# Optimization experiments

Hardware: AMD Instinct MI355X
Metric: run time of the kernel (lower is better)

The kernel has to match this reference:

```python
import jax, jax.numpy as jnp
import numpy as np

B, S, D = 2, 2048, 1024
H = 16
HD = D // H  # 64


def setup_inputs() -> dict:
    key = jax.random.key(0)
    ks = jax.random.split(key, 6)
    std = 1.0 / np.sqrt(D)
    x = jax.random.normal(ks[0], (B, S, D), dtype=jnp.float32)
    Wq = jax.random.uniform(ks[1], (D, D), jnp.float32, -std, std)
    Wk = jax.random.uniform(ks[2], (D, D), jnp.float32, -std, std)
    Wv = jax.random.uniform(ks[3], (D, D), jnp.float32, -std, std)
    Wo = jax.random.uniform(ks[4], (D, D), jnp.float32, -std, std)
    bo = jax.random.uniform(ks[5], (D,), jnp.float32, -std, std)
    return {"x": x, "Wq": Wq, "Wk": Wk, "Wv": Wv, "Wo": Wo, "bo": bo}


def reference(x, Wq, Wk, Wv, Wo, bo):
    b, n, _ = x.shape
    # project and split heads: [b, H, n, HD]
    def split_heads(y):
        return y.reshape(b, n, H, HD).transpose(0, 2, 1, 3)
    q = split_heads(jnp.einsum('bnd,ed->bne', x, Wq))
    k = split_heads(jnp.einsum('bnd,ed->bne', x, Wk))
    v = split_heads(jnp.einsum('bnd,ed->bne', x, Wv))
    scores = jnp.einsum('bhqd,bhkd->bhqk', q, k)
    causal = jnp.triu(jnp.ones((n, n), dtype=bool), k=1)
    # original masks with -inf BEFORE scaling; -inf/scale == -inf so math matches
    scores = jnp.where(causal, -jnp.inf, scores) / jnp.sqrt(jnp.asarray(HD, scores.dtype))
    attn = jax.nn.softmax(scores, axis=-1)
    ctx = jnp.einsum('bhqk,bhkd->bhqd', attn, v)
    ctx = ctx.transpose(0, 2, 1, 3).reshape(b, n, D)
    return jnp.einsum('bnd,ed->bne', ctx, Wo) + bo
```

## Files before the change

kernel.cpp:

```cpp
#include <hip/hip_runtime.h>

#define DEV __device__ __forceinline__

typedef __bf16 bf16x8 __attribute__((ext_vector_type(8)));
typedef float f32x4 __attribute__((ext_vector_type(4)));
typedef float f32x16 __attribute__((ext_vector_type(16)));
typedef unsigned u32x4 __attribute__((ext_vector_type(4)));

constexpr int S_LEN = 2048;
constexpr int DMODEL = 1024;
constexpr int NHEAD = 16;
constexpr int HDIM = 64;
constexpr int BATCH = 2;
constexpr int MROWS = BATCH * S_LEN;
constexpr float QSCALE = 0.125f * 1.44269504088896f;

DEV short f2bf(float x) {
  unsigned u = __builtin_bit_cast(unsigned, x);
  unsigned r = u + 0x7fffu + ((u >> 16) & 1u);
  return (short)(r >> 16);
}

#define MFMA16(a, b, c) __builtin_amdgcn_mfma_f32_16x16x32_bf16((a), (b), (c), 0, 0, 0)
#define MFMA32(a, b, c) __builtin_amdgcn_mfma_f32_32x32x16_bf16((a), (b), (c), 0, 0, 0)
#define GLL16(g, l)                                                                     \
  __builtin_amdgcn_global_load_lds((const __attribute__((address_space(1))) void*)(g),  \
                                   (__attribute__((address_space(3))) void*)(l), 16, 0, 0)

DEV unsigned cvt_pk_bf16(float a, float b) {
  unsigned r;
  asm("v_cvt_pk_bf16_f32 %0, %1, %2" : "=v"(r) : "v"(a), "v"(b));
  return r;
}
DEV void swap32(unsigned& a, unsigned& b) {
  asm("v_permlane32_swap_b32 %0, %1" : "+v"(a), "+v"(b));
}

__global__ void cvt_kernel(const float* __restrict__ in, short* __restrict__ out, int n) {
  int i = (blockIdx.x * blockDim.x + threadIdx.x) * 4;
  const int stride = gridDim.x * blockDim.x * 4;
  for (; i < n; i += stride) {
    float4 v = *(const float4*)&in[i];
    short4 r;
    r.x = f2bf(v.x);
    r.y = f2bf(v.y);
    r.z = f2bf(v.z);
    r.w = f2bf(v.w);
    *(short4*)&out[i] = r;
  }
}

__global__ void cvt_w4(const float* __restrict__ Wq, const float* __restrict__ Wk,
                       const float* __restrict__ Wv, const float* __restrict__ Wo,
                       short* __restrict__ out) {
  const float* src = blockIdx.y == 0 ? Wq : blockIdx.y == 1 ? Wk : blockIdx.y == 2 ? Wv : Wo;
  short* dst = out + (size_t)blockIdx.y * (DMODEL * DMODEL);
  int i = (blockIdx.x * blockDim.x + threadIdx.x) * 4;
  const int stride = gridDim.x * blockDim.x * 4;
  for (; i < DMODEL * DMODEL; i += stride) {
    float4 v = *(const float4*)&src[i];
    short4 r;
    r.x = f2bf(v.x);
    r.y = f2bf(v.y);
    r.z = f2bf(v.z);
    r.w = f2bf(v.w);
    *(short4*)&dst[i] = r;
  }
}

__global__ __launch_bounds__(256) void gemm_bt(const short* __restrict__ A,
                                               const short* __restrict__ Bt,
                                               short* __restrict__ outb,
                                               float* __restrict__ outf,
                                               const float* __restrict__ bias,
                                               const int mode) {
  constexpr int K = DMODEL;
  constexpr int N = DMODEL;
  constexpr size_t XN = (size_t)MROWS * DMODEL;
  __shared__ short As[2][128 * 64];
  __shared__ short Bs[2][128 * 64];
  const int tid = threadIdx.x;
  const int w = tid >> 6, l = tid & 63;
  const int lr = l & 15, lh = l >> 4;
  const int wr = w >> 1, wc = w & 1;
  const int tm = blockIdx.x, tn = blockIdx.y;

  const int srow = tid >> 3;
  const int ssl = tid & 7;
  const int ssg = ssl ^ (srow & 7);

  f32x4 acc[4][4] = {};

#define GSTAGE(KT, BUF)                                                             \
  {                                                                                 \
    _Pragma("unroll") for (int i = 0; i < 4; ++i) {                                 \
      const int row = i * 32 + srow;                                                \
      GLL16(A + (size_t)(tm * 128 + row) * K + (KT)*64 + ssg * 8,                   \
            &As[BUF][(i * 256 + w * 64) * 8]);                                      \
    }                                                                               \
    _Pragma("unroll") for (int i = 0; i < 4; ++i) {                                 \
      const int row = i * 32 + srow;                                                \
      GLL16(Bt + (size_t)(tn * 128 + row) * K + (KT)*64 + ssg * 8,                  \
            &Bs[BUF][(i * 256 + w * 64) * 8]);                                      \
    }                                                                               \
  }

  GSTAGE(0, 0);
  asm volatile("s_waitcnt vmcnt(0)" ::: "memory");
  __syncthreads();

  for (int kt = 0; kt < K / 64; ++kt) {
    const int buf = kt & 1;
    if (kt < K / 64 - 1) GSTAGE(kt + 1, buf ^ 1);

#pragma unroll
    for (int kh = 0; kh < 2; ++kh) {
      bf16x8 af[4], bfr[4];
#pragma unroll
      for (int mi = 0; mi < 4; ++mi) {
        const int row = wr * 64 + mi * 16 + lr;
        af[mi] = *(const bf16x8*)&As[buf][row * 64 + 8 * ((kh * 4 + lh) ^ (row & 7))];
      }
#pragma unroll
      for (int ni = 0; ni < 4; ++ni) {
        const int row = wc * 64 + ni * 16 + lr;
        bfr[ni] = *(const bf16x8*)&Bs[buf][row * 64 + 8 * ((kh * 4 + lh) ^ (row & 7))];
      }
#pragma unroll
      for (int mi = 0; mi < 4; ++mi)
#pragma unroll
        for (int ni = 0; ni < 4; ++ni)
          acc[mi][ni] = MFMA16(af[mi], bfr[ni], acc[mi][ni]);
    }

    asm volatile("s_waitcnt vmcnt(0)" ::: "memory");
    __syncthreads();
  }
#undef GSTAGE

  const int m0 = tm * 128 + wr * 64;
  const int n0 = tn * 128 + wc * 64;
  if (mode == 3) {
#pragma unroll
    for (int mi = 0; mi < 4; ++mi)
#pragma unroll
      for (int ni = 0; ni < 4; ++ni)
#pragma unroll
        for (int i = 0; i < 4; ++i) {
          const int m = m0 + mi * 16 + lh * 4 + i;
          const int e = n0 + ni * 16 + lr;
          outf[(size_t)m * N + e] = acc[mi][ni][i] + bias[e];
        }
  } else {
    const int sel = tn >> 3;
#pragma unroll
    for (int mi = 0; mi < 4; ++mi)
#pragma unroll
      for (int ni = 0; ni < 4; ++ni)
#pragma unroll
        for (int i = 0; i < 4; ++i) {
          const int m = m0 + mi * 16 + lh * 4 + i;
          const int e = n0 + ni * 16 + lr;
          const int ecol = e & (DMODEL - 1);
          const int b = m >> 11, n = m & (S_LEN - 1);
          const int h = ecol >> 6, d = ecol & (HDIM - 1);
          if (sel == 0)
            outb[((size_t)((b * NHEAD + h) * S_LEN + n)) * HDIM + d] =
                f2bf(acc[mi][ni][i] * QSCALE);
          else if (sel == 1)
            (outb + XN)[((size_t)((b * NHEAD + h) * S_LEN + n)) * HDIM + d] =
                f2bf(acc[mi][ni][i]);
          else
            (outb + 2 * XN)[((size_t)((b * NHEAD + h) * HDIM + d)) * S_LEN + n] =
                f2bf(acc[mi][ni][i]);
        }
  }
}

__global__ __launch_bounds__(256) void attn_kernel(const short* __restrict__ Qg,
                                                   const short* __restrict__ Kg,
                                                   const short* __restrict__ Vg,
                                                   short* __restrict__ ctx) {
  __shared__ alignas(16) short KV[4][8192];
  __shared__ float mls[4][32];
  const int tidx = threadIdx.x;
  const int s = tidx >> 6;
  const int l = tidx & 63;
  const int lq = l & 31;
  const int h5 = l >> 5;
  const int bid = blockIdx.x;
  const int xcd = bid & 7;
  const int j = bid >> 3;
  const int bh = xcd * 4 + (j >> 6);
  const int qi = 63 - (j & 63);
  const int qbase = qi * 32;
  const short* Qh = Qg + (size_t)bh * (S_LEN * HDIM);
  const short* Kh = Kg + (size_t)bh * (S_LEN * HDIM);
  const short* Vh = Vg + (size_t)bh * (HDIM * S_LEN);

  short* Kbase = &KV[s][0];
  short* Vbase = &KV[s][4096];
  const int r8 = l >> 3;
  const int sc = l & 7;

  bf16x8 qf[4];
#pragma unroll
  for (int cc = 0; cc < 4; ++cc)
    qf[cc] = *(const bf16x8*)&Qh[(size_t)(qbase + lq) * HDIM + cc * 16 + h5 * 8];

  f32x16 o0 = {}, o1 = {};
  float ll = 0.f;

  const int ntot = qi + 1;
  const int ts = (ntot * s) >> 2;
  const int te = (ntot * (s + 1)) >> 2;

#define STAGE(T, BUF)                                                              \
  {                                                                                \
    _Pragma("unroll") for (int i = 0; i < 4; ++i) {                                \
      const int R = i * 8 + r8;                                 \
      const int sg = sc ^ (R & 7);          \
      GLL16(Kh + (size_t)((T)*32 + R) * HDIM + sg * 8,                             \
            &Kbase[(BUF)*2048 + i * 512]);                                         \
      GLL16(Vh + (size_t)(2 * R + (sg >> 2)) * S_LEN + (T)*32 + (sg & 3) * 8,      \
            &Vbase[(BUF)*2048 + i * 512]);                                         \
    }                                                                              \
  }

  if (ts < te) STAGE(ts, 0);

  for (int t = ts; t < te; ++t) {
    const int buf = (t - ts) & 1;
    if (t + 1 < te) {
      STAGE(t + 1, buf ^ 1);
      asm volatile("s_waitcnt vmcnt(8)" ::: "memory");
    } else {
      asm volatile("s_waitcnt vmcnt(0)" ::: "memory");
    }
    const short* Ksb = &Kbase[buf * 2048];
    const short* Vsb = &Vbase[buf * 2048];

    bf16x8 kf[4];
#pragma unroll
    for (int cc = 0; cc < 4; ++cc)
      kf[cc] = *(const bf16x8*)&Ksb[lq * 64 + 8 * ((cc * 2 + h5) ^ (lq & 7))];
    f32x16 st = {};
    __builtin_amdgcn_s_setprio(1);
#pragma unroll
    for (int cc = 0; cc < 4; ++cc) st = MFMA32(kf[cc], qf[cc], st);
    __builtin_amdgcn_s_setprio(0);

    if (t == qi) {
#pragma unroll
      for (int rr = 0; rr < 16; ++rr) {
        const int crow = (rr & 3) + 8 * (rr >> 2) + 4 * h5;
        if (crow > lq) st[rr] = -__builtin_inff();
      }
    }

#pragma unroll
    for (int rr = 0; rr < 16; ++rr) {
      st[rr] = __builtin_amdgcn_exp2f(st[rr]);
      ll += st[rr];
    }

    unsigned a0 = cvt_pk_bf16(st[0], st[1]), b0 = cvt_pk_bf16(st[4], st[5]);
    unsigned a1 = cvt_pk_bf16(st[2], st[3]), b1 = cvt_pk_bf16(st[6], st[7]);
    unsigned a2 = cvt_pk_bf16(st[8], st[9]), b2 = cvt_pk_bf16(st[12], st[13]);
    unsigned a3 = cvt_pk_bf16(st[10], st[11]), b3 = cvt_pk_bf16(st[14], st[15]);
    swap32(a0, b0);
    swap32(a1, b1);
    swap32(a2, b2);
    swap32(a3, b3);
    const u32x4 pw0 = {a0, a1, b0, b1};
    const u32x4 pw1 = {a2, a3, b2, b3};
    const bf16x8 pa0 = __builtin_bit_cast(bf16x8, pw0);
    const bf16x8 pa1 = __builtin_bit_cast(bf16x8, pw1);

    const int R0 = lq >> 1, p0 = (lq & 1) * 4 + h5;
    const int R1 = 16 + (lq >> 1);
    const bf16x8 v00 = *(const bf16x8*)&Vsb[R0 * 64 + 8 * ((p0 + 0) ^ (R0 & 7))];
    const bf16x8 v01 = *(const bf16x8*)&Vsb[R0 * 64 + 8 * ((p0 + 2) ^ (R0 & 7))];
    const bf16x8 v10 = *(const bf16x8*)&Vsb[R1 * 64 + 8 * ((p0 + 0) ^ (R1 & 7))];
    const bf16x8 v11 = *(const bf16x8*)&Vsb[R1 * 64 + 8 * ((p0 + 2) ^ (R1 & 7))];
    __builtin_amdgcn_s_setprio(1);
    o0 = MFMA32(pa0, v00, o0);
    o1 = MFMA32(pa0, v10, o1);
    o0 = MFMA32(pa1, v01, o0);
    o1 = MFMA32(pa1, v11, o1);
    __builtin_amdgcn_s_setprio(0);
  }
#undef STAGE

  float* me = (float*)&KV[s][0];
#pragma unroll
  for (int rr = 0; rr < 16; ++rr) {
    const int crow = (rr & 3) + 8 * (rr >> 2) + 4 * h5;
    me[crow * 64 + lq] = o0[rr];
    me[crow * 64 + 32 + lq] = o1[rr];
  }
  ll += __shfl_xor(ll, 32);
  if (h5 == 0) mls[s][lq] = ll;
  __syncthreads();

  const float* om0 = (const float*)&KV[0][0];
  const float* om1 = (const float*)&KV[1][0];
  const float* om2 = (const float*)&KV[2][0];
  const float* om3 = (const float*)&KV[3][0];
  const int b = bh >> 4, h = bh & (NHEAD - 1);
  const int r2 = tidx >> 3;
  const int d0 = (tidx & 7) * 8;
  const float inv =
      __builtin_amdgcn_rcpf(mls[0][r2] + mls[1][r2] + mls[2][r2] + mls[3][r2]);
  const size_t base = (size_t)(b * S_LEN + qbase + r2) * DMODEL + h * HDIM + d0;
#pragma unroll
  for (int i = 0; i < 8; ++i) {
    const int o = r2 * 64 + d0 + i;
    const float v = (om0[o] + om1[o] + om2[o] + om3[o]) * inv;
    ctx[base + i] = f2bf(v);
  }
}

extern "C" void kernel_launch(void* const* d_in, const int* in_sizes, int n_in,
                              void* d_out, int out_size, void* d_ws, size_t ws_size,
                              hipStream_t stream) {
  const float* x = (const float*)d_in[0];
  const float* Wq = (const float*)d_in[1];
  const float* Wk = (const float*)d_in[2];
  const float* Wv = (const float*)d_in[3];
  const float* Wo = (const float*)d_in[4];
  const float* bo = (const float*)d_in[5];

  const size_t XN = (size_t)MROWS * DMODEL;
  const size_t WN = (size_t)DMODEL * DMODEL;

  short* ws = (short*)d_ws;
  short* xb = ws;
  short* Wqb = xb + XN;
  short* Wob = Wqb + 3 * WN;
  short* Qb = Wob + WN;
  short* Kb = Qb + XN;
  short* Vb = Kb + XN;
  short* ctxb = Vb + XN;
  if (ws_size < (5 * XN + 4 * WN) * sizeof(short)) return;

  cvt_kernel<<<2048, 256, 0, stream>>>(x, xb, (int)XN);
  cvt_w4<<<dim3(256, 4), 256, 0, stream>>>(Wq, Wk, Wv, Wo, Wqb);

  gemm_bt<<<dim3(MROWS / 128, 3 * DMODEL / 128), 256, 0, stream>>>(xb, Wqb, Qb, nullptr,
                                                                   nullptr, 4);

  attn_kernel<<<2048, 256, 0, stream>>>(Qb, Kb, Vb, ctxb);

  gemm_bt<<<dim3(MROWS / 128, DMODEL / 128), 256, 0, stream>>>(ctxb, Wob, nullptr,
                                                               (float*)d_out, bo, 3);
}
```

Measured before the change: 132.5 us.

## Split attention KV across 8 waves, add smaller-tile output GEMM, swap V MFMA operands

The attention kernel now runs 512 threads per block, so the causal KV range is split across 8 waves instead of 4, and the final combine sums 8 partial outputs. The V projection swaps the MFMA operands so each lane's accumulator lands along the sequence dimension, which makes the transposed V stores more contiguous. The output projection moves to a dedicated kernel with 64x128 tiles, doubling the block count to fill the machine better. The costs are more LDS per attention block and a heavier reduction, which may lower occupancy, plus extra kernel code to maintain.

```diff
diff --git a/kernel.cpp b/kernel.cpp
--- a/kernel.cpp
+++ b/kernel.cpp
@@ -70,12 +70,8 @@
 
 __global__ __launch_bounds__(256) void gemm_bt(const short* __restrict__ A,
                                                const short* __restrict__ Bt,
-                                               short* __restrict__ outb,
-                                               float* __restrict__ outf,
-                                               const float* __restrict__ bias,
-                                               const int mode) {
+                                               short* __restrict__ outb) {
   constexpr int K = DMODEL;
-  constexpr int N = DMODEL;
   constexpr size_t XN = (size_t)MROWS * DMODEL;
   __shared__ short As[2][128 * 64];
   __shared__ short Bs[2][128 * 64];
@@ -84,6 +80,7 @@
   const int lr = l & 15, lh = l >> 4;
   const int wr = w >> 1, wc = w & 1;
   const int tm = blockIdx.x, tn = blockIdx.y;
+  const bool vswap = (tn >= 16);
 
   const int srow = tid >> 3;
   const int ssl = tid & 7;
@@ -126,11 +123,19 @@
         const int row = wc * 64 + ni * 16 + lr;
         bfr[ni] = *(const bf16x8*)&Bs[buf][row * 64 + 8 * ((kh * 4 + lh) ^ (row & 7))];
       }
-#pragma unroll
-      for (int mi = 0; mi < 4; ++mi)
-#pragma unroll
-        for (int ni = 0; ni < 4; ++ni)
-          acc[mi][ni] = MFMA16(af[mi], bfr[ni], acc[mi][ni]);
+      if (vswap) {
+#pragma unroll
+        for (int mi = 0; mi < 4; ++mi)
+#pragma unroll
+          for (int ni = 0; ni < 4; ++ni)
+            acc[mi][ni] = MFMA16(bfr[ni], af[mi], acc[mi][ni]);
+      } else {
+#pragma unroll
+        for (int mi = 0; mi < 4; ++mi)
+#pragma unroll
+          for (int ni = 0; ni < 4; ++ni)
+            acc[mi][ni] = MFMA16(af[mi], bfr[ni], acc[mi][ni]);
+      }
     }
 
     asm volatile("s_waitcnt vmcnt(0)" ::: "memory");
@@ -140,16 +145,20 @@
 
   const int m0 = tm * 128 + wr * 64;
   const int n0 = tn * 128 + wc * 64;
-  if (mode == 3) {
+  if (vswap) {
 #pragma unroll
     for (int mi = 0; mi < 4; ++mi)
 #pragma unroll
       for (int ni = 0; ni < 4; ++ni)
 #pragma unroll
         for (int i = 0; i < 4; ++i) {
-          const int m = m0 + mi * 16 + lh * 4 + i;
-          const int e = n0 + ni * 16 + lr;
-          outf[(size_t)m * N + e] = acc[mi][ni][i] + bias[e];
+          const int e = n0 + ni * 16 + lh * 4 + i;
+          const int m = m0 + mi * 16 + lr;
+          const int ecol = e & (DMODEL - 1);
+          const int b = m >> 11, n = m & (S_LEN - 1);
+          const int h = ecol >> 6, d = ecol & (HDIM - 1);
+          (outb + 2 * XN)[((size_t)((b * NHEAD + h) * HDIM + d)) * S_LEN + n] =
+              f2bf(acc[mi][ni][i]);
         }
   } else {
     const int sel = tn >> 3;
@@ -167,22 +176,98 @@
           if (sel == 0)
             outb[((size_t)((b * NHEAD + h) * S_LEN + n)) * HDIM + d] =
                 f2bf(acc[mi][ni][i] * QSCALE);
-          else if (sel == 1)
+          else
             (outb + XN)[((size_t)((b * NHEAD + h) * S_LEN + n)) * HDIM + d] =
                 f2bf(acc[mi][ni][i]);
-          else
-            (outb + 2 * XN)[((size_t)((b * NHEAD + h) * HDIM + d)) * S_LEN + n] =
-                f2bf(acc[mi][ni][i]);
         }
   }
 }
 
-__global__ __launch_bounds__(256) void attn_kernel(const short* __restrict__ Qg,
+__global__ __launch_bounds__(256) void gemm_out(const short* __restrict__ A,
+                                                const short* __restrict__ Bt,
+                                                float* __restrict__ outf,
+                                                const float* __restrict__ bias) {
+  constexpr int K = DMODEL;
+  constexpr int N = DMODEL;
+  __shared__ short As[2][64 * 64];
+  __shared__ short Bs[2][128 * 64];
+  const int tid = threadIdx.x;
+  const int w = tid >> 6, l = tid & 63;
+  const int lr = l & 15, lh = l >> 4;
+  const int wc = w;
+  const int tm = blockIdx.x, tn = blockIdx.y;
+
+  const int srow = tid >> 3;
+  const int ssl = tid & 7;
+  const int ssg = ssl ^ (srow & 7);
+
+  f32x4 acc[4][2] = {};
+
+#define OSTAGE(KT, BUF)                                                             \
+  {                                                                                 \
+    _Pragma("unroll") for (int i = 0; i < 2; ++i) {                                 \
+      const int row = i * 32 + srow;                                                \
+      GLL16(A + (size_t)(tm * 64 + row) * K + (KT)*64 + ssg * 8,                    \
+            &As[BUF][(i * 256 + w * 64) * 8]);                                      \
+    }                                                                               \
+    _Pragma("unroll") for (int i = 0; i < 4; ++i) {                                 \
+      const int row = i * 32 + srow;                                                \
+      GLL16(Bt + (size_t)(tn * 128 + row) * K + (KT)*64 + ssg * 8,                  \
+            &Bs[BUF][(i * 256 + w * 64) * 8]);                                      \
+    }                                                                               \
+  }
+
+  OSTAGE(0, 0);
+  asm volatile("s_waitcnt vmcnt(0)" ::: "memory");
+  __syncthreads();
+
+  for (int kt = 0; kt < K / 64; ++kt) {
+    const int buf = kt & 1;
+    if (kt < K / 64 - 1) OSTAGE(kt + 1, buf ^ 1);
+
+#pragma unroll
+    for (int kh = 0; kh < 2; ++kh) {
+      bf16x8 af[4], bfr[2];
+#pragma unroll
+      for (int mi = 0; mi < 4; ++mi) {
+        const int row = mi * 16 + lr;
+        af[mi] = *(const bf16x8*)&As[buf][row * 64 + 8 * ((kh * 4 + lh) ^ (row & 7))];
+      }
+#pragma unroll
+      for (int ni = 0; ni < 2; ++ni) {
+        const int row = wc * 32 + ni * 16 + lr;
+        bfr[ni] = *(const bf16x8*)&Bs[buf][row * 64 + 8 * ((kh * 4 + lh) ^ (row & 7))];
+      }
+#pragma unroll
+      for (int mi = 0; mi < 4; ++mi)
+#pragma unroll
+        for (int ni = 0; ni < 2; ++ni)
+          acc[mi][ni] = MFMA16(af[mi], bfr[ni], acc[mi][ni]);
+    }
+
+    asm volatile("s_waitcnt vmcnt(0)" ::: "memory");
+    __syncthreads();
+  }
+#undef OSTAGE
+
+#pragma unroll
+  for (int mi = 0; mi < 4; ++mi)
+#pragma unroll
+    for (int ni = 0; ni < 2; ++ni)
+#pragma unroll
+      for (int i = 0; i < 4; ++i) {
+        const int m = tm * 64 + mi * 16 + lh * 4 + i;
+        const int e = tn * 128 + wc * 32 + ni * 16 + lr;
+        outf[(size_t)m * N + e] = acc[mi][ni][i] + bias[e];
+      }
+}
+
+__global__ __launch_bounds__(512) void attn_kernel(const short* __restrict__ Qg,
                                                    const short* __restrict__ Kg,
                                                    const short* __restrict__ Vg,
                                                    short* __restrict__ ctx) {
-  __shared__ alignas(16) short KV[4][8192];
-  __shared__ float mls[4][32];
+  __shared__ alignas(16) short KV[8][8192];
+  __shared__ float mls[8][32];
   const int tidx = threadIdx.x;
   const int s = tidx >> 6;
   const int l = tidx & 63;
@@ -212,14 +297,14 @@
   float ll = 0.f;
 
   const int ntot = qi + 1;
-  const int ts = (ntot * s) >> 2;
-  const int te = (ntot * (s + 1)) >> 2;
+  const int ts = (ntot * s) >> 3;
+  const int te = (ntot * (s + 1)) >> 3;
 
 #define STAGE(T, BUF)                                                              \
   {                                                                                \
     _Pragma("unroll") for (int i = 0; i < 4; ++i) {                                \
-      const int R = i * 8 + r8;                                 \
-      const int sg = sc ^ (R & 7);          \
+      const int R = i * 8 + r8;                                                    \
+      const int sg = sc ^ (R & 7);                                                 \
       GLL16(Kh + (size_t)((T)*32 + R) * HDIM + sg * 8,                             \
             &Kbase[(BUF)*2048 + i * 512]);                                         \
       GLL16(Vh + (size_t)(2 * R + (sg >> 2)) * S_LEN + (T)*32 + (sg & 3) * 8,      \
@@ -303,21 +388,22 @@
   if (h5 == 0) mls[s][lq] = ll;
   __syncthreads();
 
-  const float* om0 = (const float*)&KV[0][0];
-  const float* om1 = (const float*)&KV[1][0];
-  const float* om2 = (const float*)&KV[2][0];
-  const float* om3 = (const float*)&KV[3][0];
+  const float* om = (const float*)&KV[0][0];
   const int b = bh >> 4, h = bh & (NHEAD - 1);
-  const int r2 = tidx >> 3;
-  const int d0 = (tidx & 7) * 8;
-  const float inv =
-      __builtin_amdgcn_rcpf(mls[0][r2] + mls[1][r2] + mls[2][r2] + mls[3][r2]);
+  const int r2 = tidx >> 4;
+  const int d0 = (tidx & 15) * 4;
+  float lsum = 0.f;
+#pragma unroll
+  for (int ss = 0; ss < 8; ++ss) lsum += mls[ss][r2];
+  const float inv = __builtin_amdgcn_rcpf(lsum);
   const size_t base = (size_t)(b * S_LEN + qbase + r2) * DMODEL + h * HDIM + d0;
 #pragma unroll
-  for (int i = 0; i < 8; ++i) {
+  for (int i = 0; i < 4; ++i) {
     const int o = r2 * 64 + d0 + i;
-    const float v = (om0[o] + om1[o] + om2[o] + om3[o]) * inv;
-    ctx[base + i] = f2bf(v);
+    float v = 0.f;
+#pragma unroll
+    for (int ss = 0; ss < 8; ++ss) v += om[ss * 4096 + o];
+    ctx[base + i] = f2bf(v * inv);
   }
 }
 
@@ -347,11 +433,10 @@
   cvt_kernel<<<2048, 256, 0, stream>>>(x, xb, (int)XN);
   cvt_w4<<<dim3(256, 4), 256, 0, stream>>>(Wq, Wk, Wv, Wo, Wqb);
 
-  gemm_bt<<<dim3(MROWS / 128, 3 * DMODEL / 128), 256, 0, stream>>>(xb, Wqb, Qb, nullptr,
-                                                                   nullptr, 4);
-
-  attn_kernel<<<2048, 256, 0, stream>>>(Qb, Kb, Vb, ctxb);
-
-  gemm_bt<<<dim3(MROWS / 128, DMODEL / 128), 256, 0, stream>>>(ctxb, Wob, nullptr,
-                                                               (float*)d_out, bo, 3);
-}
+  gemm_bt<<<dim3(MROWS / 128, 3 * DMODEL / 128), 256, 0, stream>>>(xb, Wqb, Qb);
+
+  attn_kernel<<<2048, 512, 0, stream>>>(Qb, Kb, Vb, ctxb);
+
+  gemm_out<<<dim3(MROWS / 64, DMODEL / 128), 256, 0, stream>>>(ctxb, Wob, (float*)d_out,
+                                                               bo);
+}
```

New measurement: 125.7 us. 1.05x faster.
